# Performance work log

Hardware: AMD Instinct MI355X
Metric: run time of the kernel (lower is better)

## Reference

```python
import jax, jax.numpy as jnp
import numpy as np

N1, F_IN, E1 = 50000, 128, 1000000   # data1: 10 graphs x 5000 nodes
B, NPG = 10, 5000
N2, E2 = 199, 4000                    # data2: fixed by fc1 in-dim 9950 = 50*199
K = 50
LN_EPS = 1e-5


def setup_inputs() -> dict:
    key = jax.random.key(0)
    ks = jax.random.split(key, 24)
    s = lambda k, shape: (jax.random.normal(k, shape, jnp.float32) * 0.05)
    inp = {}
    inp["x1"] = jax.random.normal(ks[0], (N1, F_IN), jnp.float32)
    inp["edge_index1"] = jax.random.randint(ks[1], (2, E1), 0, N1, jnp.int32)
    inp["batch1"] = jnp.repeat(jnp.arange(B, dtype=jnp.int32), NPG)  # equal-size graphs
    inp["x2"] = jax.random.normal(ks[2], (N2, F_IN), jnp.float32)
    inp["edge_index2"] = jax.random.randint(ks[3], (2, E2), 0, N2, jnp.int32)
    # GNN params (shared Siamese weights). PyG SAGEConv: lin_l (aggr, has bias), lin_r (root, no bias)
    inp["w1l"] = s(ks[4], (128, F_IN)); inp["b1l"] = jnp.zeros((128,), jnp.float32)
    inp["w1r"] = s(ks[5], (128, F_IN))
    inp["w2l"] = s(ks[6], (64, 128));   inp["b2l"] = jnp.zeros((64,), jnp.float32)
    inp["w2r"] = s(ks[7], (64, 128))
    # MLP head
    inp["fc1_w"] = s(ks[8], (128, K * N2)); inp["fc1_b"] = jnp.zeros((128,), jnp.float32)
    inp["ln1_g"] = jnp.ones((128,), jnp.float32); inp["ln1_b"] = jnp.zeros((128,), jnp.float32)
    inp["fc2_w"] = s(ks[9], (64, 128)); inp["fc2_b"] = jnp.zeros((64,), jnp.float32)
    inp["ln2_g"] = jnp.ones((64,), jnp.float32); inp["ln2_b"] = jnp.zeros((64,), jnp.float32)
    inp["fc3_w"] = s(ks[10], (1, 64)); inp["fc3_b"] = jnp.zeros((1,), jnp.float32)
    return inp


def _sage(x, edge_index, wl, bl, wr, n_nodes):
    # mean aggregation of source features at target nodes, then two linears
    src, dst = edge_index[0], edge_index[1]
    msg_sum = jax.ops.segment_sum(x[src], dst, num_segments=n_nodes)
    cnt = jax.ops.segment_sum(jnp.ones((edge_index.shape[1], 1), x.dtype), dst,
                              num_segments=n_nodes)
    mean = msg_sum / jnp.maximum(cnt, 1.0)
    return mean @ wl.T + bl + x @ wr.T


def _gnn(x, ei, w1l, b1l, w1r, w2l, b2l, w2r):
    n = x.shape[0]
    h = jax.nn.relu(_sage(x, ei, w1l, b1l, w1r, n))
    return jax.nn.relu(_sage(h, ei, w2l, b2l, w2r, n))


def _layernorm(x, g, b):
    mu = jnp.mean(x, -1, keepdims=True)
    var = jnp.mean((x - mu) ** 2, -1, keepdims=True)
    return (x - mu) * jax.lax.rsqrt(var + LN_EPS) * g + b


def reference(x1, edge_index1, batch1, x2, edge_index2,
              w1l, b1l, w1r, w2l, b2l, w2r,
              fc1_w, fc1_b, ln1_g, ln1_b, fc2_w, fc2_b, ln2_g, ln2_b, fc3_w, fc3_b):
    out1 = _gnn(x1, edge_index1, w1l, b1l, w1r, w2l, b2l, w2r)   # [N1, 64]
    out2 = _gnn(x2, edge_index2, w1l, b1l, w1r, w2l, b2l, w2r)   # [N2, 64]
    # cdist p=2
    a2 = jnp.sum(out1 * out1, -1, keepdims=True)                 # [N1,1]
    b2 = jnp.sum(out2 * out2, -1)                                # [N2]
    d2 = a2 + b2[None, :] - 2.0 * (out1 @ out2.T)
    dist = jnp.sqrt(jnp.maximum(d2, 0.0))                        # [N1, N2]
    # SortAggregation(k=50): per-graph sort rows by last column (desc), take top k.
    # batch1 groups equal-size graphs contiguously -> reshape is exact dense batching.
    xb = dist.reshape(B, NPG, N2)
    order = jnp.argsort(-xb[:, :, -1], axis=1)[:, :K]            # [B, K]
    topk = jnp.take_along_axis(xb, order[:, :, None], axis=1)    # [B, K, N2]
    out = topk.reshape(B, K * N2)
    out = jax.nn.relu(_layernorm(out @ fc1_w.T + fc1_b, ln1_g, ln1_b))
    out = jax.nn.relu(_layernorm(out @ fc2_w.T + fc2_b, ln2_g, ln2_b))
    out = jax.nn.sigmoid(out @ fc3_w.T + fc3_b)                  # [B, 1]
    return out
```

## Files before the change

### kernel.cpp

```cpp
#include <hip/hip_runtime.h>
#include <math.h>

#define N1 50000
#define F_IN 128
#define E1 1000000
#define Bg 10
#define NPG 5000
#define N2 199
#define E2 4000
#define KSEL 50
#define LN_EPS 1e-5f
#define CHUNKS 16
#define CHSZ 313
#define EBT 4096
#define NB 196
#define BCAP 6144

typedef unsigned long long ull;

__global__ void k_bucket(const int* __restrict__ ei1, int* __restrict__ bcnt,
                         unsigned int* __restrict__ bed,
                         const int* __restrict__ ei2, int* __restrict__ rp2,
                         int* __restrict__ srcs2) {
  int t = threadIdx.x;
  int blk = blockIdx.x;
  const int nEdgeBlocks = (E1 + EBT - 1) / EBT;
  if (blk == nEdgeBlocks) {
    __shared__ int cnt2[N2];
    __shared__ int cur2[N2];
    const int* src = ei2;
    const int* dst = ei2 + E2;
    for (int i = t; i < N2; i += 256) cnt2[i] = 0;
    __syncthreads();
    for (int e = t; e < E2; e += 256) atomicAdd(&cnt2[dst[e]], 1);
    __syncthreads();
    if (t == 0) {
      int run = 0;
      rp2[0] = 0;
      for (int i = 0; i < N2; i++) {
        cur2[i] = run;
        run += cnt2[i];
        rp2[i + 1] = run;
      }
    }
    __syncthreads();
    for (int e = t; e < E2; e += 256) {
      int d = dst[e];
      int pos = atomicAdd(&cur2[d], 1);
      srcs2[pos] = src[e];
    }
    return;
  }
  __shared__ int hcnt[NB];
  const int* src = ei1;
  const int* dst = ei1 + E1;
  int e0 = blk * EBT;
  int e1 = min(e0 + EBT, E1);
  if (t < NB) hcnt[t] = 0;
  __syncthreads();
  for (int e = e0 + t; e < e1; e += 256) atomicAdd(&hcnt[dst[e] >> 8], 1);
  __syncthreads();
  if (t < NB) hcnt[t] = atomicAdd(&bcnt[t], hcnt[t]);
  __syncthreads();
  for (int e = e0 + t; e < e1; e += 256) {
    int d = dst[e];
    int s = src[e];
    int b = d >> 8;
    int pos = atomicAdd(&hcnt[b], 1);
    if (pos < BCAP)
      bed[(size_t)b * BCAP + pos] = ((unsigned int)(d & 255) << 16) | (unsigned int)s;
  }
}

__global__ __launch_bounds__(1024) void k_csr_bucket(
    const int* __restrict__ bcnt, const unsigned int* __restrict__ bed,
    int* __restrict__ rp, int* __restrict__ srcs) {
  __shared__ int cnt[256];
  __shared__ int cur[256];
  __shared__ int wsums[4];
  __shared__ int s_bbase;
  int b = blockIdx.x, t = threadIdx.x;
  int lane = t & 63, w = t >> 6;
  int total = min(bcnt[b], BCAP);
  if (t < 256) cnt[t] = 0;
  if (w == 0) {
    int vb = 0;
    for (int i = lane; i < b; i += 64) vb += min(bcnt[i], BCAP);
    for (int off = 32; off; off >>= 1) vb += __shfl_xor(vb, off);
    if (lane == 0) s_bbase = vb;
  }
  __syncthreads();
  const unsigned int* list = bed + (size_t)b * BCAP;
  for (int e = t; e < total; e += 1024) atomicAdd(&cnt[list[e] >> 16], 1);
  __syncthreads();
  int incl = 0, v = 0;
  if (t < 256) {
    v = cnt[t];
    int x = v;
#pragma unroll
    for (int off = 1; off < 64; off <<= 1) {
      int y = __shfl_up(x, off);
      if (lane >= off) x += y;
    }
    if (lane == 63) wsums[w] = x;
    incl = x;
  }
  __syncthreads();
  if (t < 256) {
    int pre = 0;
    for (int i = 0; i < w; i++) pre += wsums[i];
    incl += pre;
    int bbase = s_bbase;
    int node = b * 256 + t;
    if (node < N1) rp[node + 1] = bbase + incl;
    cur[t] = bbase + incl - v;
    if (b == 0 && t == 0) rp[0] = 0;
  }
  __syncthreads();
  for (int e = t; e < total; e += 1024) {
    unsigned int pe = list[e];
    int pos = atomicAdd(&cur[pe >> 16], 1);
    srcs[pos] = (int)(pe & 0xFFFFu);
  }
}

__global__ void k_aggr128(const float* __restrict__ xA, const int* __restrict__ rpA,
                          const int* __restrict__ srcsA, float* __restrict__ meanA, int nA,
                          const float* __restrict__ xB, const int* __restrict__ rpB,
                          const int* __restrict__ srcsB, float* __restrict__ meanB, int nB,
                          int blocksA) {
  int blk = blockIdx.x;
  const float* x;
  const int* rp;
  const int* srcs;
  float* mean;
  int n, nb0;
  if (blk < blocksA) { x = xA; rp = rpA; srcs = srcsA; mean = meanA; n = nA; nb0 = blk * 4; }
  else { x = xB; rp = rpB; srcs = srcsB; mean = meanB; n = nB; nb0 = (blk - blocksA) * 4; }
  int lane = threadIdx.x & 63;
  int node = nb0 + (threadIdx.x >> 6);
  if (node >= n) return;
  int s = rp[node], e = rp[node + 1];
  int half = lane >> 5;
  int sub = lane & 31;
  const float4* xp = (const float4*)x;
  float4 acc = make_float4(0.f, 0.f, 0.f, 0.f);
  int i = s;
  for (; i + 8 <= e; i += 8) {
    int s0 = srcs[i + half];
    int s1 = srcs[i + 2 + half];
    int s2 = srcs[i + 4 + half];
    int s3 = srcs[i + 6 + half];
    float4 v0 = xp[(size_t)s0 * 32 + sub];
    float4 v1 = xp[(size_t)s1 * 32 + sub];
    float4 v2 = xp[(size_t)s2 * 32 + sub];
    float4 v3 = xp[(size_t)s3 * 32 + sub];
    acc.x += (v0.x + v1.x) + (v2.x + v3.x);
    acc.y += (v0.y + v1.y) + (v2.y + v3.y);
    acc.z += (v0.z + v1.z) + (v2.z + v3.z);
    acc.w += (v0.w + v1.w) + (v2.w + v3.w);
  }
  for (; i + 2 <= e; i += 2) {
    int s0 = srcs[i + half];
    float4 v = xp[(size_t)s0 * 32 + sub];
    acc.x += v.x; acc.y += v.y; acc.z += v.z; acc.w += v.w;
  }
  if (i < e && half == 0) {
    float4 v = xp[(size_t)srcs[i] * 32 + sub];
    acc.x += v.x; acc.y += v.y; acc.z += v.z; acc.w += v.w;
  }
  acc.x += __shfl_xor(acc.x, 32);
  acc.y += __shfl_xor(acc.y, 32);
  acc.z += __shfl_xor(acc.z, 32);
  acc.w += __shfl_xor(acc.w, 32);
  if (half == 0) {
    float c = (float)((e - s) > 0 ? (e - s) : 1);
    float inv = 1.f / c;
    float4 o = make_float4(acc.x * inv, acc.y * inv, acc.z * inv, acc.w * inv);
    ((float4*)mean)[(size_t)node * 32 + sub] = o;
  }
}

__global__ void k_aggr_fused64(const float* __restrict__ zA, const int* __restrict__ rpA,
                               const int* __restrict__ srcsA, float* __restrict__ outA, int nA,
                               const float* __restrict__ zB, const int* __restrict__ rpB,
                               const int* __restrict__ srcsB, float* __restrict__ outB, int nB,
                               const float* __restrict__ bias, int blocksA) {
  int blk = blockIdx.x;
  const float* zlr;
  const int* rp;
  const int* srcs;
  float* out;
  int n, nb0;
  if (blk < blocksA) { zlr = zA; rp = rpA; srcs = srcsA; out = outA; n = nA; nb0 = blk * 4; }
  else { zlr = zB; rp = rpB; srcs = srcsB; out = outB; n = nB; nb0 = (blk - blocksA) * 4; }
  int lane = threadIdx.x & 63;
  int node = nb0 + (threadIdx.x >> 6);
  if (node >= n) return;
  int s = rp[node], e = rp[node + 1];
  int q = lane >> 4;
  int sub = lane & 15;
  const float4* zp = (const float4*)zlr;
  float4 acc = make_float4(0.f, 0.f, 0.f, 0.f);
  int i = s;
  for (; i + 8 <= e; i += 8) {
    int s0 = srcs[i + q];
    int s1 = srcs[i + 4 + q];
    float4 v0 = zp[(size_t)s0 * 32 + sub];
    float4 v1 = zp[(size_t)s1 * 32 + sub];
    acc.x += v0.x + v1.x;
    acc.y += v0.y + v1.y;
    acc.z += v0.z + v1.z;
    acc.w += v0.w + v1.w;
  }
  for (; i + 4 <= e; i += 4) {
    int s0 = srcs[i + q];
    float4 v = zp[(size_t)s0 * 32 + sub];
    acc.x += v.x; acc.y += v.y; acc.z += v.z; acc.w += v.w;
  }
  int rem = e - i;
  if (q < rem) {
    int s0 = srcs[i + q];
    float4 v = zp[(size_t)s0 * 32 + sub];
    acc.x += v.x; acc.y += v.y; acc.z += v.z; acc.w += v.w;
  }
  acc.x += __shfl_xor(acc.x, 16);
  acc.y += __shfl_xor(acc.y, 16);
  acc.z += __shfl_xor(acc.z, 16);
  acc.w += __shfl_xor(acc.w, 16);
  acc.x += __shfl_xor(acc.x, 32);
  acc.y += __shfl_xor(acc.y, 32);
  acc.z += __shfl_xor(acc.z, 32);
  acc.w += __shfl_xor(acc.w, 32);
  if (q == 0) {
    float c = (float)((e - s) > 0 ? (e - s) : 1);
    float inv = 1.f / c;
    float4 mb = ((const float4*)bias)[sub];
    float4 rt = zp[(size_t)node * 32 + 16 + sub];
    float v0 = acc.x * inv + mb.x + rt.x;
    float v1 = acc.y * inv + mb.y + rt.y;
    float v2 = acc.z * inv + mb.z + rt.z;
    float v3 = acc.w * inv + mb.w + rt.w;
    float4 o;
    o.x = v0 > 0.f ? v0 : 0.f;
    o.y = v1 > 0.f ? v1 : 0.f;
    o.z = v2 > 0.f ? v2 : 0.f;
    o.w = v3 > 0.f ? v3 : 0.f;
    ((float4*)out)[(size_t)node * 16 + sub] = o;
  }
}

__global__ __launch_bounds__(256) void k_sage_gemm128(
    const float* __restrict__ xinA, const float* __restrict__ meanA,
    float* __restrict__ outA, int nA,
    const float* __restrict__ xinB, const float* __restrict__ meanB,
    float* __restrict__ outB, int nB,
    const float* __restrict__ wl, const float* __restrict__ bl,
    const float* __restrict__ wr, int blocksA) {
  constexpr int TM = 128, TK = 32;
  constexpr int SA = TM + 4;
  constexpr int SW = 128 + 4;
  __shared__ float s_a[TK][SA];
  __shared__ float s_w[TK][SW];
  int blk = blockIdx.x;
  const float* xin;
  const float* mean;
  float* out;
  int n, m0;
  if (blk < blocksA) { xin = xinA; mean = meanA; out = outA; n = nA; m0 = blk * TM; }
  else { xin = xinB; mean = meanB; out = outB; n = nB; m0 = (blk - blocksA) * TM; }
  int t = threadIdx.x;
  int tx = t & 15, ty = t >> 4;
  int sub = t >> 3;
  int kv = (t & 7) << 2;

  float acc[8][8];
#pragma unroll
  for (int i = 0; i < 8; i++)
#pragma unroll
    for (int j = 0; j < 8; j++) acc[i][j] = 0.f;

  for (int ph = 0; ph < 2; ph++) {
    const float* A = ph ? xin : mean;
    const float* W = ph ? wr : wl;
    for (int k0 = 0; k0 < 128; k0 += TK) {
      __syncthreads();
#pragma unroll
      for (int p = 0; p < 4; p++) {
        int node = m0 + p * 32 + sub;
        float4 v = make_float4(0.f, 0.f, 0.f, 0.f);
        if (node < n) v = *(const float4*)&A[(size_t)node * 128 + k0 + kv];
        int col = p * 32 + sub;
        s_a[kv + 0][col] = v.x;
        s_a[kv + 1][col] = v.y;
        s_a[kv + 2][col] = v.z;
        s_a[kv + 3][col] = v.w;
      }
#pragma unroll
      for (int p = 0; p < 4; p++) {
        int j = p * 32 + sub;
        float4 v = *(const float4*)&W[(size_t)j * 128 + k0 + kv];
        s_w[kv + 0][j] = v.x;
        s_w[kv + 1][j] = v.y;
        s_w[kv + 2][j] = v.z;
        s_w[kv + 3][j] = v.w;
      }
      __syncthreads();
#pragma unroll 8
      for (int kk = 0; kk < TK; kk++) {
        float4 a0 = *(const float4*)&s_a[kk][ty * 8];
        float4 a1 = *(const float4*)&s_a[kk][ty * 8 + 4];
        float av[8] = {a0.x, a0.y, a0.z, a0.w, a1.x, a1.y, a1.z, a1.w};
        float4 w0 = *(const float4*)&s_w[kk][tx * 8];
        float4 w1 = *(const float4*)&s_w[kk][tx * 8 + 4];
        float wv[8] = {w0.x, w0.y, w0.z, w0.w, w1.x, w1.y, w1.z, w1.w};
#pragma unroll
        for (int i = 0; i < 8; i++)
#pragma unroll
          for (int j = 0; j < 8; j++) acc[i][j] = fmaf(av[i], wv[j], acc[i][j]);
      }
    }
  }
  float bj[8];
#pragma unroll
  for (int j = 0; j < 8; j++) bj[j] = bl[tx * 8 + j];
#pragma unroll
  for (int i = 0; i < 8; i++) {
    int node = m0 + ty * 8 + i;
    if (node < n) {
#pragma unroll
      for (int q = 0; q < 8; q += 4) {
        float v0 = acc[i][q + 0] + bj[q + 0];
        float v1 = acc[i][q + 1] + bj[q + 1];
        float v2 = acc[i][q + 2] + bj[q + 2];
        float v3 = acc[i][q + 3] + bj[q + 3];
        float4 o;
        o.x = v0 > 0.f ? v0 : 0.f;
        o.y = v1 > 0.f ? v1 : 0.f;
        o.z = v2 > 0.f ? v2 : 0.f;
        o.w = v3 > 0.f ? v3 : 0.f;
        *(float4*)&out[(size_t)node * 128 + tx * 8 + q] = o;
      }
    }
  }
}

__global__ __launch_bounds__(256) void k_lin_dual(
    const float* __restrict__ AA, float* __restrict__ zA, int nA,
    const float* __restrict__ AB, float* __restrict__ zB, int nB,
    const float* __restrict__ wl, const float* __restrict__ wr, int blocksA) {
  constexpr int TM = 128, TK = 32;
  constexpr int SA = TM + 4;
  constexpr int SW = 128 + 4;
  __shared__ float s_a[TK][SA];
  __shared__ float s_w[TK][SW];
  int blk = blockIdx.x;
  const float* A;
  float* zlr;
  int n, m0;
  if (blk < blocksA) { A = AA; zlr = zA; n = nA; m0 = blk * TM; }
  else { A = AB; zlr = zB; n = nB; m0 = (blk - blocksA) * TM; }
  int t = threadIdx.x;
  int tx = t & 15, ty = t >> 4;
  int sub = t >> 3;
  int kv = (t & 7) << 2;

  float acc[8][8];
#pragma unroll
  for (int i = 0; i < 8; i++)
#pragma unroll
    for (int j = 0; j < 8; j++) acc[i][j] = 0.f;

  for (int k0 = 0; k0 < 128; k0 += TK) {
    __syncthreads();
#pragma unroll
    for (int p = 0; p < 4; p++) {
      int node = m0 + p * 32 + sub;
      float4 v = make_float4(0.f, 0.f, 0.f, 0.f);
      if (node < n) v = *(const float4*)&A[(size_t)node * 128 + k0 + kv];
      int col = p * 32 + sub;
      s_a[kv + 0][col] = v.x;
      s_a[kv + 1][col] = v.y;
      s_a[kv + 2][col] = v.z;
      s_a[kv + 3][col] = v.w;
    }
#pragma unroll
    for (int p = 0; p < 4; p++) {
      int j = p * 32 + sub;
      const float* W = (j < 64) ? &wl[(size_t)j * 128] : &wr[(size_t)(j - 64) * 128];
      float4 v = *(const float4*)&W[k0 + kv];
      s_w[kv + 0][j] = v.x;
      s_w[kv + 1][j] = v.y;
      s_w[kv + 2][j] = v.z;
      s_w[kv + 3][j] = v.w;
    }
    __syncthreads();
#pragma unroll 8
    for (int kk = 0; kk < TK; kk++) {
      float4 a0 = *(const float4*)&s_a[kk][ty * 8];
      float4 a1 = *(const float4*)&s_a[kk][ty * 8 + 4];
      float av[8] = {a0.x, a0.y, a0.z, a0.w, a1.x, a1.y, a1.z, a1.w};
      float4 w0 = *(const float4*)&s_w[kk][tx * 8];
      float4 w1 = *(const float4*)&s_w[kk][tx * 8 + 4];
      float wv[8] = {w0.x, w0.y, w0.z, w0.w, w1.x, w1.y, w1.z, w1.w};
#pragma unroll
      for (int i = 0; i < 8; i++)
#pragma unroll
        for (int j = 0; j < 8; j++) acc[i][j] = fmaf(av[i], wv[j], acc[i][j]);
    }
  }
#pragma unroll
  for (int i = 0; i < 8; i++) {
    int node = m0 + ty * 8 + i;
    if (node < n) {
#pragma unroll
      for (int q = 0; q < 8; q += 4) {
        float4 o = make_float4(acc[i][q + 0], acc[i][q + 1], acc[i][q + 2], acc[i][q + 3]);
        *(float4*)&zlr[(size_t)node * 128 + tx * 8 + q] = o;
      }
    }
  }
}

__global__ void k_score_topk_local(const float* __restrict__ out1,
                                   const float* __restrict__ out2,
                                   ull* __restrict__ cand) {
  __shared__ ull s[512];
  __shared__ float brow[64];
  int blk = blockIdx.x;
  int b = blk >> 4, c = blk & 15;
  int t = threadIdx.x;
  if (t < 64) brow[t] = out2[198 * 64 + t];
  __syncthreads();
  const float4* b4 = (const float4*)brow;
  float b2 = 0.f;
#pragma unroll
  for (int q = 0; q < 16; q++) {
    float4 w = b4[q];
    b2 = fmaf(w.x, w.x, fmaf(w.y, w.y, fmaf(w.z, w.z, fmaf(w.w, w.w, b2))));
  }
#pragma unroll
  for (int p = 0; p < 2; p++) {
    int i = p * 256 + t;
    ull key = 0ULL;
    int gidx = c * CHSZ + i;
    if (i < CHSZ && gidx < NPG) {
      const float4* ap = (const float4*)&out1[((size_t)b * NPG + gidx) * 64];
      float dot = 0.f, a2 = 0.f;
#pragma unroll
      for (int q = 0; q < 16; q++) {
        float4 a = ap[q];
        float4 w = b4[q];
        dot = fmaf(a.x, w.x, fmaf(a.y, w.y, fmaf(a.z, w.z, fmaf(a.w, w.w, dot))));
        a2 = fmaf(a.x, a.x, fmaf(a.y, a.y, fmaf(a.z, a.z, fmaf(a.w, a.w, a2))));
      }
      float d2 = a2 + b2 - 2.f * dot;
      float sc = sqrtf(fmaxf(d2, 0.f));
      key = ((ull)__float_as_uint(sc) << 32) | (unsigned int)(~gidx);
    }
    s[i] = key;
  }
  __syncthreads();
  for (int k = 2; k <= 512; k <<= 1) {
    for (int j = k >> 1; j > 0; j >>= 1) {
#pragma unroll
      for (int p = 0; p < 2; p++) {
        int i = p * 256 + t;
        int l = i ^ j;
        if (l > i) {
          bool up = ((i & k) != 0);
          ull a = s[i], bb = s[l];
          if ((a > bb) == up) { s[i] = bb; s[l] = a; }
        }
      }
      __syncthreads();
    }
  }
  if (t < KSEL) cand[(b * CHUNKS + c) * KSEL + t] = s[t];
}

__global__ void k_topk_merge(const ull* __restrict__ cand, int* __restrict__ sel) {
  __shared__ ull s[1024];
  int b = blockIdx.x, t = threadIdx.x;
#pragma unroll
  for (int p = 0; p < 4; p++) {
    int i = p * 256 + t;
    s[i] = (i < CHUNKS * KSEL) ? cand[b * CHUNKS * KSEL + i] : 0ULL;
  }
  __syncthreads();
  for (int k = 2; k <= 1024; k <<= 1) {
    for (int j = k >> 1; j > 0; j >>= 1) {
#pragma unroll
      for (int p = 0; p < 4; p++) {
        int i = p * 256 + t;
        int l = i ^ j;
        if (l > i) {
          bool up = ((i & k) != 0);
          ull a = s[i], bb = s[l];
          if ((a > bb) == up) { s[i] = bb; s[l] = a; }
        }
      }
      __syncthreads();
    }
  }
  if (t < KSEL) {
    int gidx = (int)(~((unsigned int)s[t]));
    sel[b * KSEL + t] = b * NPG + gidx;
  }
}

__global__ void k_dist_rows(const float* __restrict__ out1, const float* __restrict__ out2,
                            const int* __restrict__ sel, float* __restrict__ D) {
  __shared__ float arow[64];
  int i = blockIdx.x;
  int t = threadIdx.x;
  int node = sel[i];
  if (t < 64) arow[t] = out1[(size_t)node * 64 + t];
  __syncthreads();
  float a2 = 0.f;
#pragma unroll
  for (int f = 0; f < 64; f++) a2 = fmaf(arow[f], arow[f], a2);
  for (int nn = t; nn < N2; nn += 256) {
    float dot = 0.f, b2 = 0.f;
#pragma unroll 8
    for (int f = 0; f < 64; f++) {
      float bv = out2[nn * 64 + f];
      dot = fmaf(arow[f], bv, dot);
      b2 = fmaf(bv, bv, b2);
    }
    float d2 = a2 + b2 - 2.f * dot;
    D[i * N2 + nn] = sqrtf(fmaxf(d2, 0.f));
  }
}

__global__ void k_fc1_dot(const float* __restrict__ D, const float* __restrict__ w,
                          float* __restrict__ h1pre) {
  constexpr int M = KSEL * N2;
  constexpr int M2 = M / 2;
  int j = blockIdx.x;
  int t = threadIdx.x;
  const float2* wp = (const float2*)(w + (size_t)j * M);
  float acc[Bg];
#pragma unroll
  for (int b = 0; b < Bg; b++) acc[b] = 0.f;
  for (int m = t; m < M2; m += 256) {
    float2 wv = wp[m];
#pragma unroll
    for (int b = 0; b < Bg; b++) {
      float2 dv = ((const float2*)(D + (size_t)b * M))[m];
      acc[b] = fmaf(dv.x, wv.x, fmaf(dv.y, wv.y, acc[b]));
    }
  }
  __shared__ float ws_[4][Bg];
  int lane = t & 63, wv_ = t >> 6;
#pragma unroll
  for (int b = 0; b < Bg; b++) {
    float v = acc[b];
    for (int off = 32; off; off >>= 1) v += __shfl_xor(v, off);
    if (lane == 0) ws_[wv_][b] = v;
  }
  __syncthreads();
  if (t < Bg) h1pre[t * 128 + j] = ws_[0][t] + ws_[1][t] + ws_[2][t] + ws_[3][t];
}

__global__ void k_fc123(const float* __restrict__ h1pre, const float* __restrict__ fc1b,
                        const float* __restrict__ g1, const float* __restrict__ be1,
                        const float* __restrict__ w2, const float* __restrict__ b2v,
                        const float* __restrict__ g2, const float* __restrict__ be2,
                        const float* __restrict__ w3, const float* __restrict__ b3,
                        float* __restrict__ out) {
  __shared__ float wsum[2];
  __shared__ float sh[128];
  int b = blockIdx.x, t = threadIdx.x;
  float acc = h1pre[b * 128 + t] + fc1b[t];
  int lane = t & 63, wv_ = t >> 6;
  float ssum = acc;
  for (int off = 32; off; off >>= 1) ssum += __shfl_xor(ssum, off);
  if (lane == 0) wsum[wv_] = ssum;
  __syncthreads();
  float mu = (wsum[0] + wsum[1]) / 128.f;
  __syncthreads();
  float d = acc - mu;
  float vv = d * d;
  for (int off = 32; off; off >>= 1) vv += __shfl_xor(vv, off);
  if (lane == 0) wsum[wv_] = vv;
  __syncthreads();
  float var = (wsum[0] + wsum[1]) / 128.f;
  float r = rsqrtf(var + LN_EPS);
  float h = d * r * g1[t] + be1[t];
  sh[t] = h > 0.f ? h : 0.f;
  __syncthreads();
  if (t < 64) {
    float a2 = b2v[t];
#pragma unroll 8
    for (int k = 0; k < 128; k++) a2 = fmaf(sh[k], w2[t * 128 + k], a2);
    float s2 = a2;
    for (int off = 32; off; off >>= 1) s2 += __shfl_xor(s2, off);
    float mu2 = s2 * (1.f / 64.f);
    float d2 = a2 - mu2;
    float vv2 = d2 * d2;
    for (int off = 32; off; off >>= 1) vv2 += __shfl_xor(vv2, off);
    float r2 = rsqrtf(vv2 * (1.f / 64.f) + LN_EPS);
    float h2 = d2 * r2 * g2[t] + be2[t];
    h2 = h2 > 0.f ? h2 : 0.f;
    float pp = h2 * w3[t];
    for (int off = 32; off; off >>= 1) pp += __shfl_xor(pp, off);
    if (t == 0) out[b] = 1.f / (1.f + expf(-(pp + b3[0])));
  }
}

extern "C" void kernel_launch(void* const* d_in, const int* in_sizes, int n_in,
                              void* d_out, int out_size, void* d_ws, size_t ws_size,
                              hipStream_t stream) {
  const float* x1 = (const float*)d_in[0];
  const int* ei1 = (const int*)d_in[1];
  const float* x2 = (const float*)d_in[3];
  const int* ei2 = (const int*)d_in[4];
  const float* w1l = (const float*)d_in[5];
  const float* b1l = (const float*)d_in[6];
  const float* w1r = (const float*)d_in[7];
  const float* w2l = (const float*)d_in[8];
  const float* b2l = (const float*)d_in[9];
  const float* w2r = (const float*)d_in[10];
  const float* fc1w = (const float*)d_in[11];
  const float* fc1b = (const float*)d_in[12];
  const float* ln1g = (const float*)d_in[13];
  const float* ln1b = (const float*)d_in[14];
  const float* fc2w = (const float*)d_in[15];
  const float* fc2b = (const float*)d_in[16];
  const float* ln2g = (const float*)d_in[17];
  const float* ln2b = (const float*)d_in[18];
  const float* fc3w = (const float*)d_in[19];
  const float* fc3b = (const float*)d_in[20];
  float* out = (float*)d_out;

  char* p = (char*)d_ws;
  auto alloc = [&](size_t bytes) {
    char* r = p;
    p += (bytes + 255) & ~(size_t)255;
    return r;
  };
  int* rp1 = (int*)alloc((N1 + 1) * 4);
  int* bcnt = (int*)alloc(NB * 4);
  unsigned int* bed = (unsigned int*)alloc((size_t)NB * BCAP * 4);
  int* srcs1 = (int*)alloc((size_t)E1 * 4);
  int* rp2 = (int*)alloc((N2 + 1) * 4);
  int* srcs2 = (int*)alloc(E2 * 4);
  float* bufMean = (float*)alloc((size_t)N1 * 128 * 4);
  float* bufH = (float*)alloc((size_t)N1 * 128 * 4);
  float* out1b = (float*)alloc((size_t)N1 * 64 * 4);
  float* mean2 = (float*)alloc((size_t)N2 * 128 * 4);
  float* h2g = (float*)alloc((size_t)N2 * 128 * 4);
  float* out2b = (float*)alloc((size_t)N2 * 64 * 4);
  int* sel = (int*)alloc(Bg * KSEL * 4);
  ull* cand = (ull*)alloc((size_t)Bg * CHUNKS * KSEL * 8);
  float* Dm = (float*)alloc((size_t)Bg * KSEL * N2 * 4);
  float* h1pre = (float*)alloc(Bg * 128 * 4);

  const int nEdgeBlocks = (E1 + EBT - 1) / EBT;
  const int aggrBlocksA = (N1 + 3) / 4;
  const int aggrBlocksB = (N2 + 3) / 4;
  const int gemmBlocksA = (N1 + 127) / 128;
  const int gemmBlocksB = (N2 + 127) / 128;

  hipMemsetAsync(bcnt, 0, NB * 4, stream);
  k_bucket<<<nEdgeBlocks + 1, 256, 0, stream>>>(ei1, bcnt, bed, ei2, rp2, srcs2);
  k_csr_bucket<<<NB, 1024, 0, stream>>>(bcnt, bed, rp1, srcs1);
  k_aggr128<<<aggrBlocksA + aggrBlocksB, 256, 0, stream>>>(
      x1, rp1, srcs1, bufMean, N1, x2, rp2, srcs2, mean2, N2, aggrBlocksA);
  k_sage_gemm128<<<gemmBlocksA + gemmBlocksB, 256, 0, stream>>>(
      x1, bufMean, bufH, N1, x2, mean2, h2g, N2, w1l, b1l, w1r, gemmBlocksA);
  k_lin_dual<<<gemmBlocksA + gemmBlocksB, 256, 0, stream>>>(
      bufH, bufMean, N1, h2g, mean2, N2, w2l, w2r, gemmBlocksA);
  k_aggr_fused64<<<aggrBlocksA + aggrBlocksB, 256, 0, stream>>>(
      bufMean, rp1, srcs1, out1b, N1, mean2, rp2, srcs2, out2b, N2, b2l, aggrBlocksA);
  k_score_topk_local<<<Bg * CHUNKS, 256, 0, stream>>>(out1b, out2b, cand);
  k_topk_merge<<<Bg, 256, 0, stream>>>(cand, sel);
  k_dist_rows<<<Bg * KSEL, 256, 0, stream>>>(out1b, out2b, sel, Dm);
  k_fc1_dot<<<128, 256, 0, stream>>>(Dm, fc1w, h1pre);
  k_fc123<<<Bg, 128, 0, stream>>>(h1pre, fc1b, ln1g, ln1b, fc2w, fc2b, ln2g, ln2b,
                                  fc3w, fc3b, out);
}
```

Measured before the change: 394.0 us.

## Fuse SAGE layer-1 GEMM with layer-2 linear and shuffle-broadcast edge indices

```diff
diff --git a/kernel.cpp b/kernel.cpp
--- a/kernel.cpp
+++ b/kernel.cpp
@@ -141,16 +141,20 @@
   int node = nb0 + (threadIdx.x >> 6);
   if (node >= n) return;
   int s = rp[node], e = rp[node + 1];
+  int deg = e - s;
   int half = lane >> 5;
   int sub = lane & 31;
   const float4* xp = (const float4*)x;
   float4 acc = make_float4(0.f, 0.f, 0.f, 0.f);
-  int i = s;
-  for (; i + 8 <= e; i += 8) {
-    int s0 = srcs[i + half];
-    int s1 = srcs[i + 2 + half];
-    int s2 = srcs[i + 4 + half];
-    int s3 = srcs[i + 6 + half];
+  int sv = 0;
+  if (s + lane < e) sv = srcs[s + lane];
+  int lim = deg < 64 ? deg : 64;
+  int i = 0;
+  for (; i + 8 <= lim; i += 8) {
+    int s0 = __shfl(sv, i + half);
+    int s1 = __shfl(sv, i + 2 + half);
+    int s2 = __shfl(sv, i + 4 + half);
+    int s3 = __shfl(sv, i + 6 + half);
     float4 v0 = xp[(size_t)s0 * 32 + sub];
     float4 v1 = xp[(size_t)s1 * 32 + sub];
     float4 v2 = xp[(size_t)s2 * 32 + sub];
@@ -160,21 +164,51 @@
     acc.z += (v0.z + v1.z) + (v2.z + v3.z);
     acc.w += (v0.w + v1.w) + (v2.w + v3.w);
   }
-  for (; i + 2 <= e; i += 2) {
-    int s0 = srcs[i + half];
+  for (; i + 2 <= lim; i += 2) {
+    int s0 = __shfl(sv, i + half);
     float4 v = xp[(size_t)s0 * 32 + sub];
     acc.x += v.x; acc.y += v.y; acc.z += v.z; acc.w += v.w;
   }
-  if (i < e && half == 0) {
-    float4 v = xp[(size_t)srcs[i] * 32 + sub];
-    acc.x += v.x; acc.y += v.y; acc.z += v.z; acc.w += v.w;
+  if (i < lim) {
+    int s0 = __shfl(sv, i);
+    if (half == 0) {
+      float4 v = xp[(size_t)s0 * 32 + sub];
+      acc.x += v.x; acc.y += v.y; acc.z += v.z; acc.w += v.w;
+    }
+    i = lim;
+  }
+  if (deg > 64) {
+    int ii = s + 64;
+    for (; ii + 8 <= e; ii += 8) {
+      int s0 = srcs[ii + half];
+      int s1 = srcs[ii + 2 + half];
+      int s2 = srcs[ii + 4 + half];
+      int s3 = srcs[ii + 6 + half];
+      float4 v0 = xp[(size_t)s0 * 32 + sub];
+      float4 v1 = xp[(size_t)s1 * 32 + sub];
+      float4 v2 = xp[(size_t)s2 * 32 + sub];
+      float4 v3 = xp[(size_t)s3 * 32 + sub];
+      acc.x += (v0.x + v1.x) + (v2.x + v3.x);
+      acc.y += (v0.y + v1.y) + (v2.y + v3.y);
+      acc.z += (v0.z + v1.z) + (v2.z + v3.z);
+      acc.w += (v0.w + v1.w) + (v2.w + v3.w);
+    }
+    for (; ii + 2 <= e; ii += 2) {
+      int s0 = srcs[ii + half];
+      float4 v = xp[(size_t)s0 * 32 + sub];
+      acc.x += v.x; acc.y += v.y; acc.z += v.z; acc.w += v.w;
+    }
+    if (ii < e && half == 0) {
+      float4 v = xp[(size_t)srcs[ii] * 32 + sub];
+      acc.x += v.x; acc.y += v.y; acc.z += v.z; acc.w += v.w;
+    }
   }
   acc.x += __shfl_xor(acc.x, 32);
   acc.y += __shfl_xor(acc.y, 32);
   acc.z += __shfl_xor(acc.z, 32);
   acc.w += __shfl_xor(acc.w, 32);
   if (half == 0) {
-    float c = (float)((e - s) > 0 ? (e - s) : 1);
+    float c = (float)(deg > 0 ? deg : 1);
     float inv = 1.f / c;
     float4 o = make_float4(acc.x * inv, acc.y * inv, acc.z * inv, acc.w * inv);
     ((float4*)mean)[(size_t)node * 32 + sub] = o;
@@ -198,14 +232,18 @@
   int node = nb0 + (threadIdx.x >> 6);
   if (node >= n) return;
   int s = rp[node], e = rp[node + 1];
+  int deg = e - s;
   int q = lane >> 4;
   int sub = lane & 15;
   const float4* zp = (const float4*)zlr;
   float4 acc = make_float4(0.f, 0.f, 0.f, 0.f);
-  int i = s;
-  for (; i + 8 <= e; i += 8) {
-    int s0 = srcs[i + q];
-    int s1 = srcs[i + 4 + q];
+  int sv = 0;
+  if (s + lane < e) sv = srcs[s + lane];
+  int lim = deg < 64 ? deg : 64;
+  int i = 0;
+  for (; i + 8 <= lim; i += 8) {
+    int s0 = __shfl(sv, i + q);
+    int s1 = __shfl(sv, i + 4 + q);
     float4 v0 = zp[(size_t)s0 * 32 + sub];
     float4 v1 = zp[(size_t)s1 * 32 + sub];
     acc.x += v0.x + v1.x;
@@ -213,16 +251,43 @@
     acc.z += v0.z + v1.z;
     acc.w += v0.w + v1.w;
   }
-  for (; i + 4 <= e; i += 4) {
-    int s0 = srcs[i + q];
+  for (; i + 4 <= lim; i += 4) {
+    int s0 = __shfl(sv, i + q);
     float4 v = zp[(size_t)s0 * 32 + sub];
     acc.x += v.x; acc.y += v.y; acc.z += v.z; acc.w += v.w;
   }
-  int rem = e - i;
-  if (q < rem) {
-    int s0 = srcs[i + q];
-    float4 v = zp[(size_t)s0 * 32 + sub];
-    acc.x += v.x; acc.y += v.y; acc.z += v.z; acc.w += v.w;
+  {
+    int rem = lim - i;
+    int s0 = __shfl(sv, i + q);
+    if (q < rem) {
+      float4 v = zp[(size_t)s0 * 32 + sub];
+      acc.x += v.x; acc.y += v.y; acc.z += v.z; acc.w += v.w;
+    }
+    i = lim;
+  }
+  if (deg > 64) {
+    int ii = s + 64;
+    for (; ii + 8 <= e; ii += 8) {
+      int s0 = srcs[ii + q];
+      int s1 = srcs[ii + 4 + q];
+      float4 v0 = zp[(size_t)s0 * 32 + sub];
+      float4 v1 = zp[(size_t)s1 * 32 + sub];
+      acc.x += v0.x + v1.x;
+      acc.y += v0.y + v1.y;
+      acc.z += v0.z + v1.z;
+      acc.w += v0.w + v1.w;
+    }
+    for (; ii + 4 <= e; ii += 4) {
+      int s0 = srcs[ii + q];
+      float4 v = zp[(size_t)s0 * 32 + sub];
+      acc.x += v.x; acc.y += v.y; acc.z += v.z; acc.w += v.w;
+    }
+    int rem = e - ii;
+    if (q < rem) {
+      int s0 = srcs[ii + q];
+      float4 v = zp[(size_t)s0 * 32 + sub];
+      acc.x += v.x; acc.y += v.y; acc.z += v.z; acc.w += v.w;
+    }
   }
   acc.x += __shfl_xor(acc.x, 16);
   acc.y += __shfl_xor(acc.y, 16);
@@ -233,7 +298,7 @@
   acc.z += __shfl_xor(acc.z, 32);
   acc.w += __shfl_xor(acc.w, 32);
   if (q == 0) {
-    float c = (float)((e - s) > 0 ? (e - s) : 1);
+    float c = (float)(deg > 0 ? deg : 1);
     float inv = 1.f / c;
     float4 mb = ((const float4*)bias)[sub];
     float4 rt = zp[(size_t)node * 32 + 16 + sub];
@@ -250,13 +315,14 @@
   }
 }
 
-__global__ __launch_bounds__(256) void k_sage_gemm128(
+__global__ __launch_bounds__(256) void k_sage_lin(
     const float* __restrict__ xinA, const float* __restrict__ meanA,
-    float* __restrict__ outA, int nA,
+    float* __restrict__ zA, int nA,
     const float* __restrict__ xinB, const float* __restrict__ meanB,
-    float* __restrict__ outB, int nB,
-    const float* __restrict__ wl, const float* __restrict__ bl,
-    const float* __restrict__ wr, int blocksA) {
+    float* __restrict__ zB, int nB,
+    const float* __restrict__ w1l, const float* __restrict__ b1l,
+    const float* __restrict__ w1r,
+    const float* __restrict__ w2l, const float* __restrict__ w2r, int blocksA) {
   constexpr int TM = 128, TK = 32;
   constexpr int SA = TM + 4;
   constexpr int SW = 128 + 4;
@@ -265,10 +331,10 @@
   int blk = blockIdx.x;
   const float* xin;
   const float* mean;
-  float* out;
+  float* zlr;
   int n, m0;
-  if (blk < blocksA) { xin = xinA; mean = meanA; out = outA; n = nA; m0 = blk * TM; }
-  else { xin = xinB; mean = meanB; out = outB; n = nB; m0 = (blk - blocksA) * TM; }
+  if (blk < blocksA) { xin = xinA; mean = meanA; zlr = zA; n = nA; m0 = blk * TM; }
+  else { xin = xinB; mean = meanB; zlr = zB; n = nB; m0 = (blk - blocksA) * TM; }
   int t = threadIdx.x;
   int tx = t & 15, ty = t >> 4;
   int sub = t >> 3;
@@ -282,7 +348,7 @@
 
   for (int ph = 0; ph < 2; ph++) {
     const float* A = ph ? xin : mean;
-    const float* W = ph ? wr : wl;
+    const float* W = ph ? w1r : w1l;
     for (int k0 = 0; k0 < 128; k0 += TK) {
       __syncthreads();
 #pragma unroll
@@ -321,73 +387,33 @@
       }
     }
   }
-  float bj[8];
-#pragma unroll
-  for (int j = 0; j < 8; j++) bj[j] = bl[tx * 8 + j];
-#pragma unroll
-  for (int i = 0; i < 8; i++) {
-    int node = m0 + ty * 8 + i;
-    if (node < n) {
-#pragma unroll
-      for (int q = 0; q < 8; q += 4) {
-        float v0 = acc[i][q + 0] + bj[q + 0];
-        float v1 = acc[i][q + 1] + bj[q + 1];
-        float v2 = acc[i][q + 2] + bj[q + 2];
-        float v3 = acc[i][q + 3] + bj[q + 3];
-        float4 o;
-        o.x = v0 > 0.f ? v0 : 0.f;
-        o.y = v1 > 0.f ? v1 : 0.f;
-        o.z = v2 > 0.f ? v2 : 0.f;
-        o.w = v3 > 0.f ? v3 : 0.f;
-        *(float4*)&out[(size_t)node * 128 + tx * 8 + q] = o;
-      }
-    }
-  }
-}
-
-__global__ __launch_bounds__(256) void k_lin_dual(
-    const float* __restrict__ AA, float* __restrict__ zA, int nA,
-    const float* __restrict__ AB, float* __restrict__ zB, int nB,
-    const float* __restrict__ wl, const float* __restrict__ wr, int blocksA) {
-  constexpr int TM = 128, TK = 32;
-  constexpr int SA = TM + 4;
-  constexpr int SW = 128 + 4;
-  __shared__ float s_a[TK][SA];
-  __shared__ float s_w[TK][SW];
-  int blk = blockIdx.x;
-  const float* A;
-  float* zlr;
-  int n, m0;
-  if (blk < blocksA) { A = AA; zlr = zA; n = nA; m0 = blk * TM; }
-  else { A = AB; zlr = zB; n = nB; m0 = (blk - blocksA) * TM; }
-  int t = threadIdx.x;
-  int tx = t & 15, ty = t >> 4;
-  int sub = t >> 3;
-  int kv = (t & 7) << 2;
-
-  float acc[8][8];
-#pragma unroll
-  for (int i = 0; i < 8; i++)
-#pragma unroll
-    for (int j = 0; j < 8; j++) acc[i][j] = 0.f;
-
+  float h[8][8];
+  {
+    float bj[8];
+#pragma unroll
+    for (int j = 0; j < 8; j++) bj[j] = b1l[tx * 8 + j];
+#pragma unroll
+    for (int i = 0; i < 8; i++)
+#pragma unroll
+      for (int j = 0; j < 8; j++) {
+        float v = acc[i][j] + bj[j];
+        h[i][j] = v > 0.f ? v : 0.f;
+        acc[i][j] = 0.f;
+      }
+  }
   for (int k0 = 0; k0 < 128; k0 += TK) {
     __syncthreads();
-#pragma unroll
-    for (int p = 0; p < 4; p++) {
-      int node = m0 + p * 32 + sub;
-      float4 v = make_float4(0.f, 0.f, 0.f, 0.f);
-      if (node < n) v = *(const float4*)&A[(size_t)node * 128 + k0 + kv];
-      int col = p * 32 + sub;
-      s_a[kv + 0][col] = v.x;
-      s_a[kv + 1][col] = v.y;
-      s_a[kv + 2][col] = v.z;
-      s_a[kv + 3][col] = v.w;
+    int txk = tx - (k0 >> 3);
+    if (txk >= 0 && txk < 4) {
+#pragma unroll
+      for (int i = 0; i < 8; i++)
+#pragma unroll
+        for (int j = 0; j < 8; j++) s_a[txk * 8 + j][ty * 8 + i] = h[i][j];
     }
 #pragma unroll
     for (int p = 0; p < 4; p++) {
       int j = p * 32 + sub;
-      const float* W = (j < 64) ? &wl[(size_t)j * 128] : &wr[(size_t)(j - 64) * 128];
+      const float* W = (j < 64) ? &w2l[(size_t)j * 128] : &w2r[(size_t)(j - 64) * 128];
       float4 v = *(const float4*)&W[k0 + kv];
       s_w[kv + 0][j] = v.x;
       s_w[kv + 1][j] = v.y;
@@ -647,10 +673,10 @@
   int* rp2 = (int*)alloc((N2 + 1) * 4);
   int* srcs2 = (int*)alloc(E2 * 4);
   float* bufMean = (float*)alloc((size_t)N1 * 128 * 4);
-  float* bufH = (float*)alloc((size_t)N1 * 128 * 4);
+  float* bufZ = (float*)alloc((size_t)N1 * 128 * 4);
   float* out1b = (float*)alloc((size_t)N1 * 64 * 4);
   float* mean2 = (float*)alloc((size_t)N2 * 128 * 4);
-  float* h2g = (float*)alloc((size_t)N2 * 128 * 4);
+  float* z2g = (float*)alloc((size_t)N2 * 128 * 4);
   float* out2b = (float*)alloc((size_t)N2 * 64 * 4);
   int* sel = (int*)alloc(Bg * KSEL * 4);
   ull* cand = (ull*)alloc((size_t)Bg * CHUNKS * KSEL * 8);
@@ -668,12 +694,10 @@
   k_csr_bucket<<<NB, 1024, 0, stream>>>(bcnt, bed, rp1, srcs1);
   k_aggr128<<<aggrBlocksA + aggrBlocksB, 256, 0, stream>>>(
       x1, rp1, srcs1, bufMean, N1, x2, rp2, srcs2, mean2, N2, aggrBlocksA);
-  k_sage_gemm128<<<gemmBlocksA + gemmBlocksB, 256, 0, stream>>>(
-      x1, bufMean, bufH, N1, x2, mean2, h2g, N2, w1l, b1l, w1r, gemmBlocksA);
-  k_lin_dual<<<gemmBlocksA + gemmBlocksB, 256, 0, stream>>>(
-      bufH, bufMean, N1, h2g, mean2, N2, w2l, w2r, gemmBlocksA);
+  k_sage_lin<<<gemmBlocksA + gemmBlocksB, 256, 0, stream>>>(
+      x1, bufMean, bufZ, N1, x2, mean2, z2g, N2, w1l, b1l, w1r, w2l, w2r, gemmBlocksA);
   k_aggr_fused64<<<aggrBlocksA + aggrBlocksB, 256, 0, stream>>>(
-      bufMean, rp1, srcs1, out1b, N1, mean2, rp2, srcs2, out2b, N2, b2l, aggrBlocksA);
+      bufZ, rp1, srcs1, out1b, N1, z2g, rp2, srcs2, out2b, N2, b2l, aggrBlocksA);
   k_score_topk_local<<<Bg * CHUNKS, 256, 0, stream>>>(out1b, out2b, cand);
   k_topk_merge<<<Bg, 256, 0, stream>>>(cand, sel);
   k_dist_rows<<<Bg * KSEL, 256, 0, stream>>>(out1b, out2b, sel, Dm);
```

Result: faster. 386.1 us (-2.0%).
